# Kernel optimization log

Measured on AMD Instinct MI355X. Metric: run time of the kernel, lower is better.

Reference implementation:

```python
import jax, jax.numpy as jnp
import numpy as np

HEADS = 8
HEAD_DIM = 32
PRE_H = 32
PRE_W = 32
SCALE = HEAD_DIM ** (-0.5)


def _relative_indices(H, W):
    # Faithful to torch loop: out[p, q] = (gy[q]-y_p+H)*W + (gx[q]-x_p+W)
    gy, gx = np.meshgrid(np.arange(H), np.arange(W), indexing='ij')
    gy = gy.reshape(-1)
    gx = gx.reshape(-1)
    idx = (gy[None, :] - gy[:, None] + H) * W + (gx[None, :] - gx[:, None] + W)
    return idx.astype(np.int32)  # [HW, HW]


def setup_inputs() -> dict:
    key = jax.random.key(0)
    ks = jax.random.split(key, 7)
    b, c, H, W = 16, 256, PRE_H, PRE_W
    dim = HEADS * HEAD_DIM  # 256
    x = jax.random.normal(ks[0], (b, c, H, W), dtype=jnp.float32)
    # nn.Linear weights: [out_features, in_features]
    Wq = jax.random.normal(ks[1], (dim, c), dtype=jnp.float32) * 0.02
    Wk = jax.random.normal(ks[2], (dim, c), dtype=jnp.float32) * 0.02
    Wv = jax.random.normal(ks[3], (dim, c), dtype=jnp.float32) * 0.02
    Wo = jax.random.normal(ks[4], (c, dim), dtype=jnp.float32) * 0.02
    bo = jax.random.normal(ks[5], (c,), dtype=jnp.float32) * 0.02
    rel_bias = jax.random.normal(ks[6], (HEADS, (2 * PRE_H - 1) * (2 * PRE_W - 1)), dtype=jnp.float32)
    rel_idx = jnp.asarray(_relative_indices(PRE_H, PRE_W))
    return {"x": x, "Wq": Wq, "Wk": Wk, "Wv": Wv, "Wo": Wo, "bo": bo,
            "rel_bias": rel_bias, "rel_idx": rel_idx}


def reference(x, Wq, Wk, Wv, Wo, bo, rel_bias, rel_idx):
    b, c, H, W = x.shape
    n = H * W
    h, d = HEADS, HEAD_DIM
    # b c h w -> b (h w) c
    xt = x.reshape(b, c, n).transpose(0, 2, 1)
    q = (xt @ Wq.T).reshape(b, n, h, d).transpose(0, 2, 1, 3)  # b h n d
    k = (xt @ Wk.T).reshape(b, n, h, d).transpose(0, 2, 1, 3)
    v = (xt @ Wv.T).reshape(b, n, h, d).transpose(0, 2, 1, 3)
    k = k * SCALE
    # gathered relative bias: [h, n, n]
    bias = rel_bias[:, rel_idx]
    attn = jnp.einsum('bhnd,bhmd->bhnm', q, k) + bias[None]
    attn = jax.nn.softmax(attn, axis=-1)
    out = jnp.einsum('bhnm,bhmd->bhnd', attn, v)
    out = out.transpose(0, 2, 1, 3).reshape(b, n, h * d)  # b n (h d)
    out = out @ Wo.T + bo
    # b (h w) c -> b c h w
    return out.transpose(0, 2, 1).reshape(b, c, H, W)
```

## Files before the change

### kernel.cpp

```cpp
#include <hip/hip_runtime.h>

#define HEADS 8
#define HDIM 32
#define NTOK 1024
#define CDIM 256
#define BATCH 16
#define ATT_SCALE 0.17677669529663687f
#define L2E 1.4426950408889634f
#define BSTR 1544

typedef __attribute__((ext_vector_type(8))) short bf16x8;
typedef __attribute__((ext_vector_type(4))) float f32x4;

__device__ __forceinline__ unsigned short f2bf(float f) {
    unsigned int u = __float_as_uint(f);
    return (unsigned short)((u + 0x7fffu + ((u >> 16) & 1u)) >> 16);
}

__device__ __forceinline__ unsigned cvt_pk_bf16(float lo, float hi) {
    unsigned r;
    asm("v_cvt_pk_bf16_f32 %0, %1, %2" : "=v"(r) : "v"(lo), "v"(hi));
    return r;
}

__global__ __launch_bounds__(256) void prep_kernel(
    const float* __restrict__ x,
    const float* __restrict__ Wq, const float* __restrict__ Wk,
    const float* __restrict__ Wv, const float* __restrict__ Wo,
    unsigned short* __restrict__ w16, unsigned short* __restrict__ xt16)
{
    const int t = threadIdx.x;
    if (blockIdx.z == 16) {
        const int which = blockIdx.y;
        const float* src = (which == 0) ? Wq : ((which == 1) ? Wk : ((which == 2) ? Wv : Wo));
        const float scale = (which == 1) ? (ATT_SCALE * L2E) : 1.0f;
        const int base = (blockIdx.x * 256 + t) * 16;
        #pragma unroll
        for (int i = 0; i < 4; ++i) {
            const int idx = base + i * 4;
            float4 v = *(const float4*)&src[idx];
            union { unsigned short h[4]; uint2 u; } pk;
            pk.h[0] = f2bf(v.x * scale); pk.h[1] = f2bf(v.y * scale);
            pk.h[2] = f2bf(v.z * scale); pk.h[3] = f2bf(v.w * scale);
            *(uint2*)&w16[(size_t)which * 65536 + idx] = pk.u;
        }
        return;
    }
    __shared__ float tile[64][65];
    const int b = blockIdx.z, ct = blockIdx.y * 64, nt = blockIdx.x * 64;
    const float* xb = x + ((size_t)b * CDIM + ct) * NTOK + nt;
    const int cc = t >> 4, n4 = (t & 15) * 4;
    #pragma unroll
    for (int i = 0; i < 4; ++i) {
        float4 v = *(const float4*)&xb[(size_t)(cc + 16 * i) * NTOK + n4];
        tile[cc + 16 * i][n4]     = v.x;
        tile[cc + 16 * i][n4 + 1] = v.y;
        tile[cc + 16 * i][n4 + 2] = v.z;
        tile[cc + 16 * i][n4 + 3] = v.w;
    }
    __syncthreads();
    const int c0 = (t & 7) * 8;
    #pragma unroll
    for (int i = 0; i < 2; ++i) {
        const int nl = (t >> 3) + 32 * i;
        union { unsigned short h[8]; uint4 u; } pk;
        #pragma unroll
        for (int j = 0; j < 8; ++j) pk.h[j] = f2bf(tile[c0 + j][nl]);
        *(uint4*)&xt16[((size_t)b * NTOK + nt + nl) * CDIM + ct + c0] = pk.u;
    }
}

__global__ __launch_bounds__(1024, 4) void qkv_kernel(
    const unsigned short* __restrict__ xt16,
    const unsigned short* __restrict__ w16,
    unsigned short* __restrict__ q16,
    unsigned short* __restrict__ k16,
    unsigned short* __restrict__ v16)
{
    const int id   = blockIdx.x;
    const int bh_i = (id & 7) * 16 + (id >> 4);
    const int tokhalf = (id >> 3) & 1;
    const int b = bh_i >> 3, h = bh_i & 7;

    const int t = threadIdx.x, wid = t >> 6, lane = t & 63;
    const int g = lane >> 4, ln = lane & 15;
    const int tr = tokhalf * 512 + wid * 32;

    const unsigned short* xb  = xt16 + (size_t)b * NTOK * CDIM;
    const unsigned short* wqh = w16 + (size_t)(h * 32) * CDIM;
    const unsigned short* wkh = w16 + 65536 + (size_t)(h * 32) * CDIM;
    const unsigned short* wvh = w16 + 2 * 65536 + (size_t)(h * 32) * CDIM;

    f32x4 aq[2][2], ak[2][2], av[2][2];
    #pragma unroll
    for (int m = 0; m < 2; ++m)
        #pragma unroll
        for (int n = 0; n < 2; ++n) {
            aq[m][n] = (f32x4){0.f, 0.f, 0.f, 0.f};
            ak[m][n] = (f32x4){0.f, 0.f, 0.f, 0.f};
            av[n][m] = (f32x4){0.f, 0.f, 0.f, 0.f};
        }
    #pragma unroll
    for (int kt = 0; kt < CDIM; kt += 32) {
        bf16x8 xf[2], wqf[2], wkf[2], wvf[2];
        #pragma unroll
        for (int m = 0; m < 2; ++m)
            xf[m] = *(const bf16x8*)&xb[(size_t)(tr + m * 16 + ln) * CDIM + kt + g * 8];
        #pragma unroll
        for (int n = 0; n < 2; ++n) {
            wqf[n] = *(const bf16x8*)&wqh[(size_t)(n * 16 + ln) * CDIM + kt + g * 8];
            wkf[n] = *(const bf16x8*)&wkh[(size_t)(n * 16 + ln) * CDIM + kt + g * 8];
            wvf[n] = *(const bf16x8*)&wvh[(size_t)(n * 16 + ln) * CDIM + kt + g * 8];
        }
        #pragma unroll
        for (int m = 0; m < 2; ++m)
            #pragma unroll
            for (int n = 0; n < 2; ++n) {
                aq[m][n] = __builtin_amdgcn_mfma_f32_16x16x32_bf16(xf[m], wqf[n], aq[m][n], 0, 0, 0);
                ak[m][n] = __builtin_amdgcn_mfma_f32_16x16x32_bf16(xf[m], wkf[n], ak[m][n], 0, 0, 0);
                av[n][m] = __builtin_amdgcn_mfma_f32_16x16x32_bf16(wvf[n], xf[m], av[n][m], 0, 0, 0);
            }
    }

    #pragma unroll
    for (int m = 0; m < 2; ++m)
        #pragma unroll
        for (int n = 0; n < 2; ++n)
            #pragma unroll
            for (int r = 0; r < 4; ++r)
                q16[((size_t)(b * NTOK + tr + m * 16 + g * 4 + r) * 8 + h) * 32 + n * 16 + ln] =
                    f2bf(aq[m][n][r]);

    unsigned short* kb16 = k16 + (size_t)(b * 8 + h) * 32768;
    const int fK = (tokhalf * 16 + wid) * 2 + (g & 1);
    #pragma unroll
    for (int m = 0; m < 2; ++m)
        #pragma unroll
        for (int n = 0; n < 2; ++n) {
            const int lhi = (2 * n + (ln >> 3)) * 16 + (m * 2 + (g >> 1)) * 4;
            #pragma unroll
            for (int r = 0; r < 4; ++r)
                kb16[fK * 512 + (lhi + r) * 8 + (ln & 7)] = f2bf(ak[m][n][r]);
        }

    unsigned short* vb16 = v16 + (size_t)(b * 8 + h) * 32768;
    #pragma unroll
    for (int n = 0; n < 2; ++n) {
        const int fV = (tokhalf * 16 + wid) * 2 + n;
        #pragma unroll
        for (int m = 0; m < 2; ++m) {
            const int lnb = (m * 2 + (ln >> 3)) * 16 + g * 4;
            #pragma unroll
            for (int r = 0; r < 4; ++r)
                vb16[fV * 512 + (lnb + r) * 8 + (ln & 7)] = f2bf(av[n][m][r]);
        }
    }
}

__global__ __launch_bounds__(1024, 4) void attn_kernel(
    const unsigned short* __restrict__ q16,
    const unsigned short* __restrict__ k16,
    const unsigned short* __restrict__ v16,
    const float* __restrict__ rel_bias,
    unsigned short* __restrict__ ao16)
{
    __shared__ __align__(16) unsigned char smem[65536 + 65536 + BSTR * 4 * 4];
    unsigned short* k_s   = (unsigned short*)smem;
    unsigned short* v_s   = (unsigned short*)(smem + 65536);
    float*          bias4 = (float*)(smem + 131072);

    const int id   = blockIdx.x;
    const int bh_i = (id & 7) * 16 + (id >> 4);
    const int half = (id >> 3) & 1;
    const int b = bh_i >> 3, h = bh_i & 7;

    const int t = threadIdx.x, wid = t >> 6, lane = t & 63;
    const int g = lane >> 4, ln = lane & 15;
    const int qb = half * 512 + wid * 32;

    const unsigned short* kbh = k16 + (size_t)(b * 8 + h) * 32768;
    const unsigned short* vbh = v16 + (size_t)(b * 8 + h) * 32768;

    bf16x8 sk[4], sv[4];
    #pragma unroll
    for (int j = 0; j < 4; ++j) {
        const int f = wid * 4 + j;
        sk[j] = *(const bf16x8*)&kbh[(size_t)f * 512 + lane * 8];
        sv[j] = *(const bf16x8*)&vbh[(size_t)f * 512 + lane * 8];
    }
    const bf16x8 aq0 = *(const bf16x8*)&q16[((size_t)(b * NTOK + qb + ln) * 8 + h) * 32 + g * 8];
    const bf16x8 aq1 = *(const bf16x8*)&q16[((size_t)(b * NTOK + qb + 16 + ln) * 8 + h) * 32 + g * 8];

    {
        const int START = 544 - 512 * half;
        const float* brow = rel_bias + (size_t)h * 3969;
        for (int i = t; i < 1540; i += 1024) {
            #pragma unroll
            for (int a = 0; a < 4; ++a)
                bias4[a * BSTR + i] = brow[START + a + i] * L2E;
        }
    }

    #pragma unroll
    for (int j = 0; j < 4; ++j) {
        const int f = wid * 4 + j;
        *(bf16x8*)&k_s[(size_t)f * 512 + lane * 8] = sk[j];
        *(bf16x8*)&v_s[(size_t)f * 512 + lane * 8] = sv[j];
    }

    __syncthreads();

    const int boffL = 512 + 8 * g - wid * 32 - ln;
    const int ba = boffL & 3;
    const float* bb = &bias4[ba * BSTR + (boffL - ba)];
    const unsigned short* kfp = k_s + lane * 8;
    const unsigned short* vfp = v_s + lane * 8;

    f32x4 o00 = {0.f,0.f,0.f,0.f}, o01 = {0.f,0.f,0.f,0.f};
    f32x4 o10 = {0.f,0.f,0.f,0.f}, o11 = {0.f,0.f,0.f,0.f};
    f32x4 ls0 = {0.f,0.f,0.f,0.f}, ls1 = {0.f,0.f,0.f,0.f};
    const short one_bf = (short)0x3F80;
    const bf16x8 ones = {one_bf,one_bf,one_bf,one_bf,one_bf,one_bf,one_bf,one_bf};

    bf16x8 kf0 = *(const bf16x8*)&kfp[0];
    bf16x8 kf1 = *(const bf16x8*)&kfp[512];
    f32x4  cA0 = *(const f32x4*)&bb[0];
    f32x4  cA1 = *(const f32x4*)&bb[4];
    f32x4  cB0 = *(const f32x4*)&bb[-16];
    f32x4  cB1 = *(const f32x4*)&bb[-12];

    for (int kb = 0; kb < NTOK; kb += 32) {
        const int fi = (kb >> 5) * 2;
        const bf16x8 vA0 = *(const bf16x8*)&vfp[fi * 512];
        const bf16x8 vA1 = *(const bf16x8*)&vfp[(fi + 1) * 512];
        const int kn = (kb + 32) & (NTOK - 1);
        const int fn = (kn >> 5) * 2;
        const bf16x8 nk0 = *(const bf16x8*)&kfp[fn * 512];
        const bf16x8 nk1 = *(const bf16x8*)&kfp[(fn + 1) * 512];
        const f32x4  nA0 = *(const f32x4*)&bb[kn];
        const f32x4  nA1 = *(const f32x4*)&bb[kn + 4];
        const f32x4  nB0 = *(const f32x4*)&bb[kn - 16];
        const f32x4  nB1 = *(const f32x4*)&bb[kn - 12];

        __builtin_amdgcn_s_setprio(1);
        f32x4 s00 = __builtin_amdgcn_mfma_f32_16x16x32_bf16(kf0, aq0, cA0, 0, 0, 0);
        f32x4 s01 = __builtin_amdgcn_mfma_f32_16x16x32_bf16(kf1, aq0, cA1, 0, 0, 0);
        f32x4 s10 = __builtin_amdgcn_mfma_f32_16x16x32_bf16(kf0, aq1, cB0, 0, 0, 0);
        f32x4 s11 = __builtin_amdgcn_mfma_f32_16x16x32_bf16(kf1, aq1, cB1, 0, 0, 0);
        __builtin_amdgcn_s_setprio(0);

        union { unsigned u4[4]; bf16x8 v; } ap0, ap1;
        ap0.u4[0] = cvt_pk_bf16(__builtin_amdgcn_exp2f(s00[0]), __builtin_amdgcn_exp2f(s00[1]));
        ap0.u4[1] = cvt_pk_bf16(__builtin_amdgcn_exp2f(s00[2]), __builtin_amdgcn_exp2f(s00[3]));
        ap0.u4[2] = cvt_pk_bf16(__builtin_amdgcn_exp2f(s01[0]), __builtin_amdgcn_exp2f(s01[1]));
        ap0.u4[3] = cvt_pk_bf16(__builtin_amdgcn_exp2f(s01[2]), __builtin_amdgcn_exp2f(s01[3]));
        ap1.u4[0] = cvt_pk_bf16(__builtin_amdgcn_exp2f(s10[0]), __builtin_amdgcn_exp2f(s10[1]));
        ap1.u4[1] = cvt_pk_bf16(__builtin_amdgcn_exp2f(s10[2]), __builtin_amdgcn_exp2f(s10[3]));
        ap1.u4[2] = cvt_pk_bf16(__builtin_amdgcn_exp2f(s11[0]), __builtin_amdgcn_exp2f(s11[1]));
        ap1.u4[3] = cvt_pk_bf16(__builtin_amdgcn_exp2f(s11[2]), __builtin_amdgcn_exp2f(s11[3]));

        __builtin_amdgcn_s_setprio(1);
        o00 = __builtin_amdgcn_mfma_f32_16x16x32_bf16(ap0.v, vA0, o00, 0, 0, 0);
        o01 = __builtin_amdgcn_mfma_f32_16x16x32_bf16(ap0.v, vA1, o01, 0, 0, 0);
        ls0 = __builtin_amdgcn_mfma_f32_16x16x32_bf16(ap0.v, ones, ls0, 0, 0, 0);
        o10 = __builtin_amdgcn_mfma_f32_16x16x32_bf16(ap1.v, vA0, o10, 0, 0, 0);
        o11 = __builtin_amdgcn_mfma_f32_16x16x32_bf16(ap1.v, vA1, o11, 0, 0, 0);
        ls1 = __builtin_amdgcn_mfma_f32_16x16x32_bf16(ap1.v, ones, ls1, 0, 0, 0);
        __builtin_amdgcn_s_setprio(0);

        kf0 = nk0; kf1 = nk1;
        cA0 = nA0; cA1 = nA1; cB0 = nB0; cB1 = nB1;
    }

    #pragma unroll
    for (int r = 0; r < 4; ++r) {
        float i0 = 1.f / ls0[r], i1 = 1.f / ls1[r];
        o00[r] *= i0; o01[r] *= i0;
        o10[r] *= i1; o11[r] *= i1;
    }

    __syncthreads();
    unsigned short (*otr)[32][40] = (unsigned short(*)[32][40])smem;
    #pragma unroll
    for (int r = 0; r < 4; ++r) {
        otr[wid][g * 4 + r][ln]           = f2bf(o00[r]);
        otr[wid][g * 4 + r][16 + ln]      = f2bf(o01[r]);
        otr[wid][16 + g * 4 + r][ln]      = f2bf(o10[r]);
        otr[wid][16 + g * 4 + r][16 + ln] = f2bf(o11[r]);
    }
    const int row = lane >> 1;
    const int ch  = (lane & 1) * 16;
    uint4 st0 = *(uint4*)&otr[wid][row][ch];
    uint4 st1 = *(uint4*)&otr[wid][row][ch + 8];
    unsigned short* dst = &ao16[((size_t)b * NTOK + qb + row) * CDIM + h * HDIM + ch];
    *(uint4*)dst     = st0;
    *(uint4*)&dst[8] = st1;
}

__global__ __launch_bounds__(256) void outproj_kernel(
    const unsigned short* __restrict__ ao16,
    const unsigned short* __restrict__ wo16,
    const float* __restrict__ bo,
    float* __restrict__ y)
{
    const int id   = blockIdx.x;
    const int b    = (id & 7) * 2 + ((id >> 3) & 1);
    const int rest = id >> 4;
    const int ct   = (rest & 3) * 64;
    const int pt   = (rest >> 2) * 128;
    const int t = threadIdx.x, wid = t >> 6, lane = t & 63;
    const int g = lane >> 4, ln = lane & 15;
    const int cb2 = ct + (wid & 1) * 32;
    const int pb  = pt + (wid >> 1) * 64;
    const unsigned short* ab = ao16 + (size_t)b * NTOK * CDIM;

    f32x4 acc[2][4];
    #pragma unroll
    for (int n = 0; n < 2; ++n)
        #pragma unroll
        for (int m = 0; m < 4; ++m) acc[n][m] = (f32x4){0.f, 0.f, 0.f, 0.f};

    #pragma unroll
    for (int kt = 0; kt < CDIM; kt += 32) {
        bf16x8 aw[2], bx[4];
        #pragma unroll
        for (int n = 0; n < 2; ++n)
            aw[n] = *(const bf16x8*)&wo16[(size_t)(cb2 + n * 16 + ln) * CDIM + kt + g * 8];
        #pragma unroll
        for (int m = 0; m < 4; ++m)
            bx[m] = *(const bf16x8*)&ab[(size_t)(pb + m * 16 + ln) * CDIM + kt + g * 8];
        #pragma unroll
        for (int n = 0; n < 2; ++n)
            #pragma unroll
            for (int m = 0; m < 4; ++m)
                acc[n][m] = __builtin_amdgcn_mfma_f32_16x16x32_bf16(aw[n], bx[m], acc[n][m], 0, 0, 0);
    }
    #pragma unroll
    for (int n = 0; n < 2; ++n)
        #pragma unroll
        for (int r = 0; r < 4; ++r) {
            const int c = cb2 + n * 16 + g * 4 + r;
            const float bias = bo[c];
            #pragma unroll
            for (int m = 0; m < 4; ++m)
                y[((size_t)b * CDIM + c) * NTOK + pb + m * 16 + ln] = acc[n][m][r] + bias;
        }
}

extern "C" void kernel_launch(void* const* d_in, const int* in_sizes, int n_in,
                              void* d_out, int out_size, void* d_ws, size_t ws_size,
                              hipStream_t stream) {
    const float* x        = (const float*)d_in[0];
    const float* Wq       = (const float*)d_in[1];
    const float* Wk       = (const float*)d_in[2];
    const float* Wv       = (const float*)d_in[3];
    const float* Wo       = (const float*)d_in[4];
    const float* bo       = (const float*)d_in[5];
    const float* rel_bias = (const float*)d_in[6];
    (void)in_sizes; (void)n_in; (void)ws_size; (void)out_size;

    unsigned short* ws16 = (unsigned short*)d_ws;
    unsigned short* xt16 = ws16;
    unsigned short* ao16 = ws16;
    unsigned short* w16  = ws16 + (size_t)4 * 1024 * 1024;
    unsigned short* q16  = w16 + 4 * 65536;
    unsigned short* k16  = q16 + (size_t)4 * 1024 * 1024;
    unsigned short* v16  = k16 + (size_t)4 * 1024 * 1024;
    float* y = (float*)d_out;

    prep_kernel<<<dim3(16, 4, 17), 256, 0, stream>>>(x, Wq, Wk, Wv, Wo, w16, xt16);
    qkv_kernel<<<256, 1024, 0, stream>>>(xt16, w16, q16, k16, v16);
    attn_kernel<<<256, 1024, 0, stream>>>(q16, k16, v16, rel_bias, ao16);
    outproj_kernel<<<512, 256, 0, stream>>>(ao16, w16 + 3 * 65536, bo, y);
}
```

Before: 158.0 us.

## Fuse x transpose and bf16 conversion into QKV kernel via shared-memory staging

Removes the separate pass that transposed x into a bf16 token-major buffer. The QKV kernel now loads fp32 x tiles directly into shared memory per 32-channel slice and converts them to bf16 MFMA fragments in-register, with the prep kernel reduced to weight conversion only. This saves a full write and read of the transposed activation buffer, but each block (one per batch, head and token half) now re-reads and converts the same x slice that the other seven head blocks also read. It also adds two barriers per k-step and a moved workspace layout.

```diff
diff --git a/kernel.cpp b/kernel.cpp
--- a/kernel.cpp
+++ b/kernel.cpp
@@ -8,6 +8,7 @@
 #define ATT_SCALE 0.17677669529663687f
 #define L2E 1.4426950408889634f
 #define BSTR 1544
+#define XSTR 514
 
 typedef __attribute__((ext_vector_type(8))) short bf16x8;
 typedef __attribute__((ext_vector_type(4))) float f32x4;
@@ -23,60 +24,36 @@
     return r;
 }
 
-__global__ __launch_bounds__(256) void prep_kernel(
-    const float* __restrict__ x,
+__global__ __launch_bounds__(256) void prepw_kernel(
     const float* __restrict__ Wq, const float* __restrict__ Wk,
     const float* __restrict__ Wv, const float* __restrict__ Wo,
-    unsigned short* __restrict__ w16, unsigned short* __restrict__ xt16)
+    unsigned short* __restrict__ w16)
 {
     const int t = threadIdx.x;
-    if (blockIdx.z == 16) {
-        const int which = blockIdx.y;
-        const float* src = (which == 0) ? Wq : ((which == 1) ? Wk : ((which == 2) ? Wv : Wo));
-        const float scale = (which == 1) ? (ATT_SCALE * L2E) : 1.0f;
-        const int base = (blockIdx.x * 256 + t) * 16;
-        #pragma unroll
-        for (int i = 0; i < 4; ++i) {
-            const int idx = base + i * 4;
-            float4 v = *(const float4*)&src[idx];
-            union { unsigned short h[4]; uint2 u; } pk;
-            pk.h[0] = f2bf(v.x * scale); pk.h[1] = f2bf(v.y * scale);
-            pk.h[2] = f2bf(v.z * scale); pk.h[3] = f2bf(v.w * scale);
-            *(uint2*)&w16[(size_t)which * 65536 + idx] = pk.u;
-        }
-        return;
-    }
-    __shared__ float tile[64][65];
-    const int b = blockIdx.z, ct = blockIdx.y * 64, nt = blockIdx.x * 64;
-    const float* xb = x + ((size_t)b * CDIM + ct) * NTOK + nt;
-    const int cc = t >> 4, n4 = (t & 15) * 4;
+    const int which = blockIdx.y;
+    const float* src = (which == 0) ? Wq : ((which == 1) ? Wk : ((which == 2) ? Wv : Wo));
+    const float scale = (which == 1) ? (ATT_SCALE * L2E) : 1.0f;
+    const int base = (blockIdx.x * 256 + t) * 16;
     #pragma unroll
     for (int i = 0; i < 4; ++i) {
-        float4 v = *(const float4*)&xb[(size_t)(cc + 16 * i) * NTOK + n4];
-        tile[cc + 16 * i][n4]     = v.x;
-        tile[cc + 16 * i][n4 + 1] = v.y;
-        tile[cc + 16 * i][n4 + 2] = v.z;
-        tile[cc + 16 * i][n4 + 3] = v.w;
-    }
-    __syncthreads();
-    const int c0 = (t & 7) * 8;
-    #pragma unroll
-    for (int i = 0; i < 2; ++i) {
-        const int nl = (t >> 3) + 32 * i;
-        union { unsigned short h[8]; uint4 u; } pk;
-        #pragma unroll
-        for (int j = 0; j < 8; ++j) pk.h[j] = f2bf(tile[c0 + j][nl]);
-        *(uint4*)&xt16[((size_t)b * NTOK + nt + nl) * CDIM + ct + c0] = pk.u;
+        const int idx = base + i * 4;
+        float4 v = *(const float4*)&src[idx];
+        union { unsigned short h[4]; uint2 u; } pk;
+        pk.h[0] = f2bf(v.x * scale); pk.h[1] = f2bf(v.y * scale);
+        pk.h[2] = f2bf(v.z * scale); pk.h[3] = f2bf(v.w * scale);
+        *(uint2*)&w16[(size_t)which * 65536 + idx] = pk.u;
     }
 }
 
 __global__ __launch_bounds__(1024, 4) void qkv_kernel(
-    const unsigned short* __restrict__ xt16,
+    const float* __restrict__ x,
     const unsigned short* __restrict__ w16,
     unsigned short* __restrict__ q16,
     unsigned short* __restrict__ k16,
     unsigned short* __restrict__ v16)
 {
+    __shared__ __align__(16) float lx[32 * XSTR];
+
     const int id   = blockIdx.x;
     const int bh_i = (id & 7) * 16 + (id >> 4);
     const int tokhalf = (id >> 3) & 1;
@@ -84,9 +61,10 @@
 
     const int t = threadIdx.x, wid = t >> 6, lane = t & 63;
     const int g = lane >> 4, ln = lane & 15;
-    const int tr = tokhalf * 512 + wid * 32;
-
-    const unsigned short* xb  = xt16 + (size_t)b * NTOK * CDIM;
+    const int trl = wid * 32;
+    const int tok0 = tokhalf * 512;
+
+    const float* xb = x + (size_t)b * CDIM * NTOK;
     const unsigned short* wqh = w16 + (size_t)(h * 32) * CDIM;
     const unsigned short* wkh = w16 + 65536 + (size_t)(h * 32) * CDIM;
     const unsigned short* wvh = w16 + 2 * 65536 + (size_t)(h * 32) * CDIM;
@@ -100,12 +78,31 @@
             ak[m][n] = (f32x4){0.f, 0.f, 0.f, 0.f};
             av[n][m] = (f32x4){0.f, 0.f, 0.f, 0.f};
         }
-    #pragma unroll
+
+    const int scc = t >> 7;
+    const int sn0 = (t & 127) * 4;
+
     for (int kt = 0; kt < CDIM; kt += 32) {
-        bf16x8 xf[2], wqf[2], wkf[2], wvf[2];
-        #pragma unroll
-        for (int m = 0; m < 2; ++m)
-            xf[m] = *(const bf16x8*)&xb[(size_t)(tr + m * 16 + ln) * CDIM + kt + g * 8];
+        if (kt) __syncthreads();
+        #pragma unroll
+        for (int p = 0; p < 4; ++p) {
+            const int cc = scc + 8 * p;
+            const float4 v = *(const float4*)&xb[(size_t)(kt + cc) * NTOK + tok0 + sn0];
+            *(float2*)&lx[cc * XSTR + sn0]     = make_float2(v.x, v.y);
+            *(float2*)&lx[cc * XSTR + sn0 + 2] = make_float2(v.z, v.w);
+        }
+        __syncthreads();
+        bf16x8 xf[2];
+        #pragma unroll
+        for (int m = 0; m < 2; ++m) {
+            const float* col = &lx[(size_t)(g * 8) * XSTR + trl + m * 16 + ln];
+            union { unsigned u4[4]; bf16x8 v; } pk;
+            #pragma unroll
+            for (int p = 0; p < 4; ++p)
+                pk.u4[p] = cvt_pk_bf16(col[(2 * p) * XSTR], col[(2 * p + 1) * XSTR]);
+            xf[m] = pk.v;
+        }
+        bf16x8 wqf[2], wkf[2], wvf[2];
         #pragma unroll
         for (int n = 0; n < 2; ++n) {
             wqf[n] = *(const bf16x8*)&wqh[(size_t)(n * 16 + ln) * CDIM + kt + g * 8];
@@ -122,6 +119,7 @@
             }
     }
 
+    const int tr = tok0 + trl;
     #pragma unroll
     for (int m = 0; m < 2; ++m)
         #pragma unroll
@@ -360,16 +358,15 @@
     (void)in_sizes; (void)n_in; (void)ws_size; (void)out_size;
 
     unsigned short* ws16 = (unsigned short*)d_ws;
-    unsigned short* xt16 = ws16;
-    unsigned short* ao16 = ws16;
-    unsigned short* w16  = ws16 + (size_t)4 * 1024 * 1024;
-    unsigned short* q16  = w16 + 4 * 65536;
+    unsigned short* w16  = ws16;
+    unsigned short* q16  = ws16 + 4 * 65536;
     unsigned short* k16  = q16 + (size_t)4 * 1024 * 1024;
     unsigned short* v16  = k16 + (size_t)4 * 1024 * 1024;
+    unsigned short* ao16 = v16 + (size_t)4 * 1024 * 1024;
     float* y = (float*)d_out;
 
-    prep_kernel<<<dim3(16, 4, 17), 256, 0, stream>>>(x, Wq, Wk, Wv, Wo, w16, xt16);
-    qkv_kernel<<<256, 1024, 0, stream>>>(xt16, w16, q16, k16, v16);
+    prepw_kernel<<<dim3(16, 4), 256, 0, stream>>>(Wq, Wk, Wv, Wo, w16);
+    qkv_kernel<<<256, 1024, 0, stream>>>(x, w16, q16, k16, v16);
     attn_kernel<<<256, 1024, 0, stream>>>(q16, k16, v16, rel_bias, ao16);
     outproj_kernel<<<512, 256, 0, stream>>>(ao16, w16 + 3 * 65536, bo, y);
 }
```

Measured after the change: 157.0 us, median of 2. About the same (-0.6%).
